# Kernel tuning notes

Hardware: AMD Instinct MI355X
Metric: run time of the kernel (lower is better)

## Reference

```python
import jax, jax.numpy as jnp
import numpy as np

# ---- static config ----
B, H, W, C = 32, 64, 64, 256
WS, SHIFT, NH = 8, 4, 8
HD = C // NH
N = WS * WS  # tokens per window
NW = (H // WS) * (W // WS)
EPS = 1e-5


def _relative_position_index(ws):
    ch, cw = np.meshgrid(np.arange(ws), np.arange(ws), indexing='ij')
    coords = np.stack([ch, cw]).reshape(2, -1)          # (2, N)
    rel = coords[:, :, None] - coords[:, None, :]        # (2, N, N)
    rel = rel.transpose(1, 2, 0)
    rel[:, :, 0] += ws - 1
    rel[:, :, 1] += ws - 1
    rel[:, :, 0] *= 2 * ws - 1
    return jnp.asarray(rel.sum(-1))                      # (N, N) int


def _shifted_window_mask(h, w, ws, shift):
    img = np.zeros((h, w))
    slices = (slice(0, -ws), slice(-ws, -shift), slice(-shift, None))
    cnt = 0
    for hs in slices:
        for wsl in slices:
            img[hs, wsl] = cnt
            cnt += 1
    mw = img.reshape(h // ws, ws, w // ws, ws).transpose(0, 2, 1, 3).reshape(-1, ws * ws)
    diff = mw[:, None, :] - mw[:, :, None]
    return jnp.asarray(np.where(diff != 0, -100.0, 0.0).astype(np.float32))  # (nW, N, N)


REL_IDX = _relative_position_index(WS)
ATTN_MASK = _shifted_window_mask(H, W, WS, SHIFT)


def _layernorm(x, g, b):
    mu = jnp.mean(x, axis=-1, keepdims=True)
    var = jnp.mean(jnp.square(x - mu), axis=-1, keepdims=True)
    return (x - mu) * jax.lax.rsqrt(var + EPS) * g + b


def _window_partition(x):  # (B,H,W,C) -> (B*nW, N, C)
    x = x.reshape(B, H // WS, WS, W // WS, WS, C)
    return x.transpose(0, 1, 3, 2, 4, 5).reshape(-1, N, C)


def _window_reverse(win):  # (B*nW, N, C) -> (B,H,W,C)
    x = win.reshape(B, H // WS, W // WS, WS, WS, C)
    return x.transpose(0, 1, 3, 2, 4, 5).reshape(B, H, W, C)


def setup_inputs() -> dict:
    key = jax.random.key(0)
    ks = jax.random.split(key, 6)
    s = lambda fan_in: 1.0 / np.sqrt(fan_in)
    return {
        'x': jax.random.normal(ks[0], (B, H * W, C), jnp.float32),
        'norm1_g': jnp.ones((C,), jnp.float32),
        'norm1_b': jnp.zeros((C,), jnp.float32),
        'qkv_w': jax.random.normal(ks[1], (C, 3 * C), jnp.float32) * s(C),
        'qkv_b': jnp.zeros((3 * C,), jnp.float32),
        'proj_w': jax.random.normal(ks[2], (C, C), jnp.float32) * s(C),
        'proj_b': jnp.zeros((C,), jnp.float32),
        'bias_table': jax.random.normal(ks[3], ((2 * WS - 1) ** 2, NH), jnp.float32) * 0.02,
        'norm2_g': jnp.ones((C,), jnp.float32),
        'norm2_b': jnp.zeros((C,), jnp.float32),
        'fc1_w': jax.random.normal(ks[4], (C, 4 * C), jnp.float32) * s(C),
        'fc1_b': jnp.zeros((4 * C,), jnp.float32),
        'fc2_w': jax.random.normal(ks[5], (4 * C, C), jnp.float32) * s(4 * C),
        'fc2_b': jnp.zeros((C,), jnp.float32),
    }


def reference(x, norm1_g, norm1_b, qkv_w, qkv_b, proj_w, proj_b, bias_table,
              norm2_g, norm2_b, fc1_w, fc1_b, fc2_w, fc2_b):
    shortcut = x
    h = _layernorm(x, norm1_g, norm1_b).reshape(B, H, W, C)
    # cyclic shift
    h = jnp.roll(h, shift=(-SHIFT, -SHIFT), axis=(1, 2))
    xw = _window_partition(h)                               # (Bw, N, C), Bw = B*nW
    # window attention
    qkv = xw @ qkv_w + qkv_b                                 # (Bw, N, 3C)
    qkv = qkv.reshape(-1, N, 3, NH, HD).transpose(2, 0, 3, 1, 4)
    q, k, v = qkv[0], qkv[1], qkv[2]                         # (Bw, NH, N, HD)
    attn = jnp.einsum('whnd,whmd->whnm', q * (HD ** -0.5), k)
    rpb = bias_table[REL_IDX.reshape(-1)].reshape(N, N, NH).transpose(2, 0, 1)
    attn = attn + rpb[None]
    attn = attn.reshape(B, NW, NH, N, N) + ATTN_MASK[None, :, None]
    attn = jax.nn.softmax(attn.reshape(-1, NH, N, N), axis=-1)
    out = jnp.einsum('whnm,whmd->whnd', attn, v)
    out = out.transpose(0, 2, 1, 3).reshape(-1, N, C)
    out = out @ proj_w + proj_b
    # reverse windows + shift back
    h = _window_reverse(out)
    h = jnp.roll(h, shift=(SHIFT, SHIFT), axis=(1, 2)).reshape(B, H * W, C)
    x = shortcut + h
    # MLP with pre-norm residual
    m = _layernorm(x, norm2_g, norm2_b)
    m = jax.nn.gelu(m @ fc1_w + fc1_b, approximate=False) @ fc2_w + fc2_b
    return x + m
```

## Files before the change

### kernel.cpp

```cpp
#include <hip/hip_runtime.h>
#include <hip/hip_bf16.h>


typedef __bf16 bf16;
typedef __bf16 bf16x8 __attribute__((ext_vector_type(8)));
typedef __bf16 bf16x4 __attribute__((ext_vector_type(4)));
typedef float  f32x4  __attribute__((ext_vector_type(4)));

#define M_TOK 131072

#define GLDS(gp, lp)                                                                   \
    __builtin_amdgcn_global_load_lds(                                                  \
        (const __attribute__((address_space(1))) unsigned int*)(gp),                   \
        (__attribute__((address_space(3))) unsigned int*)(lp), 16, 0, 0)

__global__ __launch_bounds__(256) void transpose_w(const float* __restrict__ src,
                                                   bf16* __restrict__ dst,
                                                   int K, int N) {
    int idx = blockIdx.x * 256 + threadIdx.x;
    int k = idx / N, n = idx - k * N;
    dst[(size_t)n * K + k] = (bf16)src[idx];
}

__global__ __launch_bounds__(256) void build_rpb(const float* __restrict__ bt,
                                                 float* __restrict__ rpb) {
    int idx = blockIdx.x * 256 + threadIdx.x;
    int h = idx >> 12, n = (idx >> 6) & 63, m = idx & 63;
    int ridx = ((n >> 3) - (m >> 3) + 7) * 15 + ((n & 7) - (m & 7) + 7);
    rpb[idx] = bt[ridx * 8 + h];
}

template <int PERM>
__global__ __launch_bounds__(256) void ln_k(const float* __restrict__ x,
                                            const float* __restrict__ g,
                                            const float* __restrict__ bb,
                                            bf16* __restrict__ dst) {
    int t = blockIdx.x * 4 + (threadIdx.x >> 6);
    int lane = threadIdx.x & 63;
    size_t src;
    if (PERM) {
        int w = t >> 6, n = t & 63;
        int b = w >> 6, nw = w & 63;
        int r = ((nw >> 3) * 8 + (n >> 3) + 4) & 63;
        int c = ((nw & 7) * 8 + (n & 7) + 4) & 63;
        src = ((size_t)b * 4096 + r * 64 + c) * 256;
    } else {
        src = (size_t)t * 256;
    }
    float4 v = *(const float4*)&x[src + lane * 4];
    float s = v.x + v.y + v.z + v.w;
    float sq = v.x * v.x + v.y * v.y + v.z * v.z + v.w * v.w;
#pragma unroll
    for (int off = 1; off < 64; off <<= 1) {
        s += __shfl_xor(s, off);
        sq += __shfl_xor(sq, off);
    }
    float mean = s * (1.0f / 256.0f);
    float var = sq * (1.0f / 256.0f) - mean * mean;
    float rstd = rsqrtf(var + 1e-5f);
    float4 gg = *(const float4*)&g[lane * 4];
    float4 bv = *(const float4*)&bb[lane * 4];
    bf16x4 o;
    o[0] = (bf16)((v.x - mean) * rstd * gg.x + bv.x);
    o[1] = (bf16)((v.y - mean) * rstd * gg.y + bv.y);
    o[2] = (bf16)((v.z - mean) * rstd * gg.z + bv.z);
    o[3] = (bf16)((v.w - mean) * rstd * gg.w + bv.w);
    *(bf16x4*)&dst[(size_t)t * 256 + lane * 4] = o;
}

__device__ __forceinline__ float fast_gelu(float v) {
    float t = v * v;
    float w = __builtin_fmaf(0.044715f * t, v, v);
    float e = __expf(-1.5957691216057308f * w);
    return v * __builtin_amdgcn_rcpf(1.0f + e);
}

template <int NDIM, int KDIM, int EPI>
__global__ __launch_bounds__(256) void gemm_k(const bf16* __restrict__ A,
                                              const bf16* __restrict__ Bt,
                                              const float* __restrict__ bias,
                                              bf16* __restrict__ outb,
                                              float* __restrict__ outf,
                                              const float* __restrict__ resid) {
    __shared__ __align__(16) bf16 SH[16384];
    constexpr int NBN = NDIM / 128;
    constexpr int NK = KDIM / 32;
    const int tid = threadIdx.x;
    const int nwg = gridDim.x;
    const int flat = blockIdx.x;
    const int cpx = nwg >> 3;
    const int orig = (flat & 7) * cpx + (flat >> 3);
    const int bm = orig / NBN, bn = orig % NBN;

    const int lane = tid & 63, wid = tid >> 6;
    const int wr = wid >> 1, wc = wid & 1;
    const int lhi = lane >> 4, llo = lane & 15;

    f32x4 acc[4][4];
#pragma unroll
    for (int i = 0; i < 4; i++)
#pragma unroll
        for (int j = 0; j < 4; j++) acc[i][j] = f32x4{0.f, 0.f, 0.f, 0.f};

    const int srow = wid * 32 + (lane >> 2);
    const int scol = (((lane & 3) - ((lane >> 3) & 3)) & 3) * 8;
    const bf16* Ap = A + (size_t)(bm * 128 + srow) * KDIM + scol;
    const bf16* Bp = Bt + (size_t)(bn * 128 + srow) * KDIM + scol;
    bf16* Al0 = SH + wid * 1024;
    bf16* Al1 = SH + 4096 + wid * 1024;
    bf16* Bl0 = SH + 8192 + wid * 1024;
    bf16* Bl1 = SH + 12288 + wid * 1024;
    const int gsw = ((lhi + (llo >> 1)) & 3) * 8;

#define STAGE(Adst, Bdst)                                                              \
    do {                                                                               \
        GLDS(Ap, (Adst));                                                              \
        GLDS(Ap + 16 * KDIM, (Adst) + 16 * 32);                                        \
        GLDS(Bp, (Bdst));                                                              \
        GLDS(Bp + 16 * KDIM, (Bdst) + 16 * 32);                                        \
        Ap += 32;                                                                      \
        Bp += 32;                                                                      \
    } while (0)

#define COMPUTE(buf)                                                                   \
    do {                                                                               \
        bf16x8 af[4], bfr[4];                                                          \
        _Pragma("unroll") for (int mi = 0; mi < 4; mi++) af[mi] =                      \
            *(const bf16x8*)&SH[(buf)*4096 + (wr * 64 + mi * 16 + llo) * 32 + gsw];    \
        _Pragma("unroll") for (int ni = 0; ni < 4; ni++) bfr[ni] =                     \
            *(const bf16x8*)&SH[8192 + (buf)*4096 + (wc * 64 + ni * 16 + llo) * 32 +   \
                                gsw];                                                  \
        _Pragma("unroll") for (int mi = 0; mi < 4; mi++)                               \
            _Pragma("unroll") for (int ni = 0; ni < 4; ni++) acc[mi][ni] =             \
                __builtin_amdgcn_mfma_f32_16x16x32_bf16(bfr[ni], af[mi],               \
                                                        acc[mi][ni], 0, 0, 0);         \
    } while (0)

#define WAIT_VM_N_BAR                                                                  \
    asm volatile("s_waitcnt vmcnt(4)" ::: "memory");                                   \
    __builtin_amdgcn_s_barrier();                                                      \
    __builtin_amdgcn_sched_barrier(0)

#define END_PHASE                                                                      \
    asm volatile("s_waitcnt lgkmcnt(0)" ::: "memory");                                 \
    __builtin_amdgcn_s_barrier();                                                      \
    __builtin_amdgcn_sched_barrier(0)

    STAGE(Al0, Bl0);
    for (int ks = 0; ks < NK - 2; ks += 2) {
        STAGE(Al1, Bl1);
        WAIT_VM_N_BAR;
        COMPUTE(0);
        END_PHASE;
        STAGE(Al0, Bl0);
        WAIT_VM_N_BAR;
        COMPUTE(1);
        END_PHASE;
    }
    STAGE(Al1, Bl1);
    WAIT_VM_N_BAR;
    COMPUTE(0);
    asm volatile("s_waitcnt vmcnt(0)" ::: "memory");
    __builtin_amdgcn_s_barrier();
    __builtin_amdgcn_sched_barrier(0);
    COMPUTE(1);

#undef STAGE
#undef COMPUTE
#undef WAIT_VM_N_BAR
#undef END_PHASE

    __syncthreads();

    char* shb = (char*)SH;
    if constexpr (EPI == 0 || EPI == 2) {
#pragma unroll
        for (int ni = 0; ni < 4; ni++) {
            const int lcol = wc * 64 + ni * 16 + lhi * 4;
            const float4 b4 = *(const float4*)&bias[bn * 128 + lcol];
#pragma unroll
            for (int mi = 0; mi < 4; mi++) {
                const int ltok = wr * 64 + mi * 16 + llo;
                float v0 = acc[mi][ni][0] + b4.x;
                float v1 = acc[mi][ni][1] + b4.y;
                float v2 = acc[mi][ni][2] + b4.z;
                float v3 = acc[mi][ni][3] + b4.w;
                bf16x4 o;
                if constexpr (EPI == 2) {
                    o[0] = (bf16)fast_gelu(v0); o[1] = (bf16)fast_gelu(v1);
                    o[2] = (bf16)fast_gelu(v2); o[3] = (bf16)fast_gelu(v3);
                } else {
                    o[0] = (bf16)v0; o[1] = (bf16)v1; o[2] = (bf16)v2; o[3] = (bf16)v3;
                }
                const int u2 = (lcol >> 3) ^ (ltok & 15);
                *(bf16x4*)(shb + ltok * 256 + u2 * 16 + (lcol & 7) * 2) = o;
            }
        }
        __syncthreads();
        const int j = lane & 15;
#pragma unroll
        for (int rnd = 0; rnd < 8; rnd++) {
            const int ltok = wid * 32 + rnd * 4 + (lane >> 4);
            const int u2 = j ^ (ltok & 15);
            bf16x8 v = *(const bf16x8*)(shb + ltok * 256 + u2 * 16);
            *(bf16x8*)&outb[(size_t)(bm * 128 + ltok) * NDIM + bn * 128 + j * 8] = v;
        }
    } else {
#pragma unroll
        for (int p = 0; p < 2; p++) {
            if (wc == p) {
#pragma unroll
                for (int ni = 0; ni < 4; ni++) {
                    const int lcolh = ni * 16 + lhi * 4;
                    const float4 b4 = *(const float4*)&bias[bn * 128 + p * 64 + lcolh];
#pragma unroll
                    for (int mi = 0; mi < 4; mi++) {
                        const int ltok = wr * 64 + mi * 16 + llo;
                        float4 o = {acc[mi][ni][0] + b4.x, acc[mi][ni][1] + b4.y,
                                    acc[mi][ni][2] + b4.z, acc[mi][ni][3] + b4.w};
                        const int u2 = (lcolh >> 2) ^ (ltok & 15);
                        *(float4*)(shb + ltok * 256 + u2 * 16) = o;
                    }
                }
            }
            __syncthreads();
            const int j = lane & 15;
#pragma unroll
            for (int rnd = 0; rnd < 8; rnd++) {
                const int ltok = wid * 32 + rnd * 4 + (lane >> 4);
                const int u2 = j ^ (ltok & 15);
                float4 v = *(const float4*)(shb + ltok * 256 + u2 * 16);
                const int gcol = bn * 128 + p * 64 + j * 4;
                const int grow = bm * 128 + ltok;
                if constexpr (EPI == 1) {
                    int w = grow >> 6, n = grow & 63;
                    int b = w >> 6, nw = w & 63;
                    int rr = ((nw >> 3) * 8 + (n >> 3) + 4) & 63;
                    int cc = ((nw & 7) * 8 + (n & 7) + 4) & 63;
                    size_t dst = ((size_t)b * 4096 + rr * 64 + cc) * 256 + gcol;
                    float4 rs = *(const float4*)&resid[dst];
                    float4 o = {rs.x + v.x, rs.y + v.y, rs.z + v.z, rs.w + v.w};
                    *(float4*)&outf[dst] = o;
                } else {
                    size_t dst = (size_t)grow * NDIM + gcol;
                    float4 cur = *(const float4*)&outf[dst];
                    float4 o = {cur.x + v.x, cur.y + v.y, cur.z + v.z, cur.w + v.w};
                    *(float4*)&outf[dst] = o;
                }
            }
            if (p == 0) __syncthreads();
        }
    }
}

__device__ __forceinline__ int regid3(int p) { return p < 56 ? 0 : (p < 60 ? 1 : 2); }

__global__ __launch_bounds__(256) void attn_k(const bf16* __restrict__ qkv,
                                              const float* __restrict__ rpb,
                                              bf16* __restrict__ aout) {
    __shared__ __align__(16) bf16 Pl[4][64 * 80];
    const int wid = threadIdx.x >> 6, lane = threadIdx.x & 63;
    const int lhi = lane >> 4, llo = lane & 15;
    const int wh = blockIdx.x * 4 + wid;
    const int w = wh >> 3, h = wh & 7;
    const bf16* base = qkv + (size_t)w * (64 * 768);

    bf16x8 qf[4], kf[4];
#pragma unroll
    for (int i = 0; i < 4; i++)
        qf[i] = *(const bf16x8*)(base + (i * 16 + llo) * 768 + h * 32 + lhi * 8);
#pragma unroll
    for (int i = 0; i < 4; i++)
        kf[i] = *(const bf16x8*)(base + (i * 16 + llo) * 768 + 256 + h * 32 + lhi * 8);
    f32x4 s[4][4];
#pragma unroll
    for (int mi = 0; mi < 4; mi++)
#pragma unroll
        for (int ni = 0; ni < 4; ni++) {
            s[mi][ni] = f32x4{0.f, 0.f, 0.f, 0.f};
            s[mi][ni] =
                __builtin_amdgcn_mfma_f32_16x16x32_bf16(qf[mi], kf[ni], s[mi][ni], 0, 0, 0);
        }

    const int nw = w & 63;
    const int pr0 = (nw >> 3) * 8, pc0 = (nw & 7) * 8;
    int creg[4];
#pragma unroll
    for (int ni = 0; ni < 4; ni++) {
        int m = ni * 16 + llo;
        creg[ni] = regid3(pr0 + (m >> 3)) * 3 + regid3(pc0 + (m & 7));
    }
    float rmax[4][4], rsum[4][4];
#pragma unroll
    for (int mi = 0; mi < 4; mi++)
#pragma unroll
        for (int r = 0; r < 4; r++) {
            int n = mi * 16 + lhi * 4 + r;
            int rreg = regid3(pr0 + (n >> 3)) * 3 + regid3(pc0 + (n & 7));
            float mx = -1e30f;
#pragma unroll
            for (int ni = 0; ni < 4; ni++) {
                int m = ni * 16 + llo;
                float sv = s[mi][ni][r] * 0.17677669529663687f + rpb[(h * 64 + n) * 64 + m] +
                           (rreg == creg[ni] ? 0.0f : -100.0f);
                s[mi][ni][r] = sv;
                mx = fmaxf(mx, sv);
            }
            rmax[mi][r] = mx;
        }
#pragma unroll
    for (int off = 1; off < 16; off <<= 1)
#pragma unroll
        for (int mi = 0; mi < 4; mi++)
#pragma unroll
            for (int r = 0; r < 4; r++)
                rmax[mi][r] = fmaxf(rmax[mi][r], __shfl_xor(rmax[mi][r], off));
#pragma unroll
    for (int mi = 0; mi < 4; mi++)
#pragma unroll
        for (int r = 0; r < 4; r++) {
            float a = 0.f;
#pragma unroll
            for (int ni = 0; ni < 4; ni++) {
                float p = __expf(s[mi][ni][r] - rmax[mi][r]);
                s[mi][ni][r] = p;
                a += p;
            }
            rsum[mi][r] = a;
        }
#pragma unroll
    for (int off = 1; off < 16; off <<= 1)
#pragma unroll
        for (int mi = 0; mi < 4; mi++)
#pragma unroll
            for (int r = 0; r < 4; r++) rsum[mi][r] += __shfl_xor(rsum[mi][r], off);

    bf16* P = Pl[wid];
#pragma unroll
    for (int mi = 0; mi < 4; mi++)
#pragma unroll
        for (int r = 0; r < 4; r++) {
            float rinv = 1.0f / rsum[mi][r];
            int row = mi * 16 + lhi * 4 + r;
#pragma unroll
            for (int ni = 0; ni < 4; ni++)
                P[row * 80 + ni * 16 + llo] = (bf16)(s[mi][ni][r] * rinv);
        }

    f32x4 o[4][2];
#pragma unroll
    for (int mi = 0; mi < 4; mi++)
#pragma unroll
        for (int ni = 0; ni < 2; ni++) o[mi][ni] = f32x4{0.f, 0.f, 0.f, 0.f};
#pragma unroll
    for (int kc = 0; kc < 2; kc++) {
        bf16x8 pf[4], vf[2];
#pragma unroll
        for (int mi = 0; mi < 4; mi++)
            pf[mi] = *(const bf16x8*)(P + (mi * 16 + llo) * 80 + kc * 32 + lhi * 8);
#pragma unroll
        for (int ni = 0; ni < 2; ni++)
#pragma unroll
            for (int j = 0; j < 8; j++)
                vf[ni][j] = base[(kc * 32 + lhi * 8 + j) * 768 + 512 + h * 32 + ni * 16 + llo];
#pragma unroll
        for (int mi = 0; mi < 4; mi++)
#pragma unroll
            for (int ni = 0; ni < 2; ni++)
                o[mi][ni] =
                    __builtin_amdgcn_mfma_f32_16x16x32_bf16(pf[mi], vf[ni], o[mi][ni], 0, 0, 0);
    }
#pragma unroll
    for (int mi = 0; mi < 4; mi++)
#pragma unroll
        for (int ni = 0; ni < 2; ni++)
#pragma unroll
            for (int r = 0; r < 4; r++) {
                int row = mi * 16 + lhi * 4 + r;
                aout[(size_t)(w * 64 + row) * 256 + h * 32 + ni * 16 + llo] =
                    (bf16)o[mi][ni][r];
            }
}

extern "C" void kernel_launch(void* const* d_in, const int* in_sizes, int n_in,
                              void* d_out, int out_size, void* d_ws, size_t ws_size,
                              hipStream_t stream) {
    const float* x      = (const float*)d_in[0];
    const float* n1g    = (const float*)d_in[1];
    const float* n1b    = (const float*)d_in[2];
    const float* qkv_w  = (const float*)d_in[3];
    const float* qkv_b  = (const float*)d_in[4];
    const float* proj_w = (const float*)d_in[5];
    const float* proj_b = (const float*)d_in[6];
    const float* btab   = (const float*)d_in[7];
    const float* n2g    = (const float*)d_in[8];
    const float* n2b    = (const float*)d_in[9];
    const float* fc1_w  = (const float*)d_in[10];
    const float* fc1_b  = (const float*)d_in[11];
    const float* fc2_w  = (const float*)d_in[12];
    const float* fc2_b  = (const float*)d_in[13];
    float* out = (float*)d_out;
    char* ws = (char*)d_ws;

    constexpr size_t o_xw   = 0;
    constexpr size_t o_qkv  = 67108864ull;
    constexpr size_t o_attn = 268435456ull;
    constexpr size_t o_g    = 0;
    constexpr size_t o_h    = 268435456ull;
    constexpr size_t o_wq   = 335544320ull;
    constexpr size_t o_wp   = o_wq + 393216;
    constexpr size_t o_w1   = o_wp + 131072;
    constexpr size_t o_w2   = o_w1 + 524288;
    constexpr size_t o_rpb  = o_w2 + 524288;

    bf16* XW   = (bf16*)(ws + o_xw);
    bf16* QKV  = (bf16*)(ws + o_qkv);
    bf16* ATTN = (bf16*)(ws + o_attn);
    bf16* G    = (bf16*)(ws + o_g);
    bf16* Hb   = (bf16*)(ws + o_h);
    bf16* WQ   = (bf16*)(ws + o_wq);
    bf16* WP   = (bf16*)(ws + o_wp);
    bf16* W1   = (bf16*)(ws + o_w1);
    bf16* W2   = (bf16*)(ws + o_w2);
    float* RPB = (float*)(ws + o_rpb);

    dim3 blk(256);
    transpose_w<<<768, blk, 0, stream>>>(qkv_w, WQ, 256, 768);
    transpose_w<<<256, blk, 0, stream>>>(proj_w, WP, 256, 256);
    transpose_w<<<1024, blk, 0, stream>>>(fc1_w, W1, 256, 1024);
    transpose_w<<<1024, blk, 0, stream>>>(fc2_w, W2, 1024, 256);
    build_rpb<<<128, blk, 0, stream>>>(btab, RPB);

    ln_k<1><<<M_TOK / 4, blk, 0, stream>>>(x, n1g, n1b, XW);
    gemm_k<768, 256, 0><<<6 * 1024, blk, 0, stream>>>(XW, WQ, qkv_b, QKV, nullptr, nullptr);
    attn_k<<<4096, blk, 0, stream>>>(QKV, RPB, ATTN);
    gemm_k<256, 256, 1><<<2 * 1024, blk, 0, stream>>>(ATTN, WP, proj_b, nullptr, out, x);
    ln_k<0><<<M_TOK / 4, blk, 0, stream>>>(out, n2g, n2b, Hb);
    gemm_k<1024, 256, 2><<<8 * 1024, blk, 0, stream>>>(Hb, W1, fc1_b, G, nullptr, nullptr);
    gemm_k<256, 1024, 3><<<2 * 1024, blk, 0, stream>>>(G, W2, fc2_b, nullptr, out, nullptr);
}
```

Measured before the change: 615.9 us.

## Deepen GEMM LDS pipeline from double to triple buffering

Changes the GEMM main loop from a two-stage to a three-stage global-to-LDS prefetch pipeline, issuing two K-steps ahead and waiting with vmcnt(8). This is meant to hide more global load latency behind MFMA work. The cost is a larger LDS footprint (48KB instead of 32KB), which may reduce occupancy, and a runtime buffer index in place of fixed unrolled buffers.

```diff
diff --git a/kernel.cpp b/kernel.cpp
--- a/kernel.cpp
+++ b/kernel.cpp
@@ -82,9 +82,10 @@
                                               bf16* __restrict__ outb,
                                               float* __restrict__ outf,
                                               const float* __restrict__ resid) {
-    __shared__ __align__(16) bf16 SH[16384];
+    __shared__ __align__(16) bf16 SH[24576];
     constexpr int NBN = NDIM / 128;
     constexpr int NK = KDIM / 32;
+    static_assert(NK >= 3, "pipeline needs >=3 K-steps");
     const int tid = threadIdx.x;
     const int nwg = gridDim.x;
     const int flat = blockIdx.x;
@@ -106,38 +107,36 @@
     const int scol = (((lane & 3) - ((lane >> 3) & 3)) & 3) * 8;
     const bf16* Ap = A + (size_t)(bm * 128 + srow) * KDIM + scol;
     const bf16* Bp = Bt + (size_t)(bn * 128 + srow) * KDIM + scol;
-    bf16* Al0 = SH + wid * 1024;
-    bf16* Al1 = SH + 4096 + wid * 1024;
-    bf16* Bl0 = SH + 8192 + wid * 1024;
-    bf16* Bl1 = SH + 12288 + wid * 1024;
     const int gsw = ((lhi + (llo >> 1)) & 3) * 8;
 
-#define STAGE(Adst, Bdst)                                                              \
+#define STAGE(bufidx)                                                                  \
     do {                                                                               \
-        GLDS(Ap, (Adst));                                                              \
-        GLDS(Ap + 16 * KDIM, (Adst) + 16 * 32);                                        \
-        GLDS(Bp, (Bdst));                                                              \
-        GLDS(Bp + 16 * KDIM, (Bdst) + 16 * 32);                                        \
+        bf16* Al = SH + (bufidx)*4096 + wid * 1024;                                    \
+        bf16* Bl = SH + 12288 + (bufidx)*4096 + wid * 1024;                            \
+        GLDS(Ap, Al);                                                                  \
+        GLDS(Ap + 16 * KDIM, Al + 16 * 32);                                            \
+        GLDS(Bp, Bl);                                                                  \
+        GLDS(Bp + 16 * KDIM, Bl + 16 * 32);                                            \
         Ap += 32;                                                                      \
         Bp += 32;                                                                      \
     } while (0)
 
-#define COMPUTE(buf)                                                                   \
+#define COMPUTE(bufidx)                                                                \
     do {                                                                               \
+        const int ab = (bufidx)*4096;                                                  \
         bf16x8 af[4], bfr[4];                                                          \
         _Pragma("unroll") for (int mi = 0; mi < 4; mi++) af[mi] =                      \
-            *(const bf16x8*)&SH[(buf)*4096 + (wr * 64 + mi * 16 + llo) * 32 + gsw];    \
+            *(const bf16x8*)&SH[ab + (wr * 64 + mi * 16 + llo) * 32 + gsw];            \
         _Pragma("unroll") for (int ni = 0; ni < 4; ni++) bfr[ni] =                     \
-            *(const bf16x8*)&SH[8192 + (buf)*4096 + (wc * 64 + ni * 16 + llo) * 32 +   \
-                                gsw];                                                  \
+            *(const bf16x8*)&SH[12288 + ab + (wc * 64 + ni * 16 + llo) * 32 + gsw];    \
         _Pragma("unroll") for (int mi = 0; mi < 4; mi++)                               \
             _Pragma("unroll") for (int ni = 0; ni < 4; ni++) acc[mi][ni] =             \
                 __builtin_amdgcn_mfma_f32_16x16x32_bf16(bfr[ni], af[mi],               \
                                                         acc[mi][ni], 0, 0, 0);         \
     } while (0)
 
-#define WAIT_VM_N_BAR                                                                  \
-    asm volatile("s_waitcnt vmcnt(4)" ::: "memory");                                   \
+#define WAITBAR(N)                                                                     \
+    asm volatile("s_waitcnt vmcnt(" #N ")" ::: "memory");                              \
     __builtin_amdgcn_s_barrier();                                                      \
     __builtin_amdgcn_sched_barrier(0)
 
@@ -146,28 +145,29 @@
     __builtin_amdgcn_s_barrier();                                                      \
     __builtin_amdgcn_sched_barrier(0)
 
-    STAGE(Al0, Bl0);
-    for (int ks = 0; ks < NK - 2; ks += 2) {
-        STAGE(Al1, Bl1);
-        WAIT_VM_N_BAR;
-        COMPUTE(0);
+    STAGE(0);
+    STAGE(1);
+    STAGE(2);
+    int buf = 0;
+    for (int i = 0; i + 3 < NK; ++i) {
+        WAITBAR(8);
+        COMPUTE(buf);
         END_PHASE;
-        STAGE(Al0, Bl0);
-        WAIT_VM_N_BAR;
-        COMPUTE(1);
-        END_PHASE;
-    }
-    STAGE(Al1, Bl1);
-    WAIT_VM_N_BAR;
-    COMPUTE(0);
-    asm volatile("s_waitcnt vmcnt(0)" ::: "memory");
-    __builtin_amdgcn_s_barrier();
-    __builtin_amdgcn_sched_barrier(0);
-    COMPUTE(1);
+        STAGE(buf);
+        buf = (buf == 2) ? 0 : buf + 1;
+    }
+    WAITBAR(8);
+    COMPUTE(buf);
+    buf = (buf == 2) ? 0 : buf + 1;
+    WAITBAR(4);
+    COMPUTE(buf);
+    buf = (buf == 2) ? 0 : buf + 1;
+    WAITBAR(0);
+    COMPUTE(buf);
 
 #undef STAGE
 #undef COMPUTE
-#undef WAIT_VM_N_BAR
+#undef WAITBAR
 #undef END_PHASE
 
     __syncthreads();
```

Measured after the change: 604.1 us. No clear change (-1.9%).

## Load GEMM operand fragments directly from global memory into registers

Applied to the files above, without the earlier changes.

Replaces the LDS-staged, double-buffered global_load_lds pipeline in the GEMM main loop with direct per-wave global loads of MFMA fragments into registers, prefetching the next K-slice while computing the current one. This removes LDS traffic and the per-step barriers. In exchange, each tile row is fetched separately by every wave that uses it (the A tile twice, the B tile twice), with no sharing through LDS. The 16-byte global loads per lane are also strided across rows, which lowers coalescing and relies on L1/L2 hits.

```diff
diff --git a/kernel.cpp b/kernel.cpp
--- a/kernel.cpp
+++ b/kernel.cpp
@@ -8,11 +8,6 @@
 typedef float  f32x4  __attribute__((ext_vector_type(4)));
 
 #define M_TOK 131072
-
-#define GLDS(gp, lp)                                                                   \
-    __builtin_amdgcn_global_load_lds(                                                  \
-        (const __attribute__((address_space(1))) unsigned int*)(gp),                   \
-        (__attribute__((address_space(3))) unsigned int*)(lp), 16, 0, 0)
 
 __global__ __launch_bounds__(256) void transpose_w(const float* __restrict__ src,
                                                    bf16* __restrict__ dst,
@@ -102,76 +97,43 @@
 #pragma unroll
         for (int j = 0; j < 4; j++) acc[i][j] = f32x4{0.f, 0.f, 0.f, 0.f};
 
-    const int srow = wid * 32 + (lane >> 2);
-    const int scol = (((lane & 3) - ((lane >> 3) & 3)) & 3) * 8;
-    const bf16* Ap = A + (size_t)(bm * 128 + srow) * KDIM + scol;
-    const bf16* Bp = Bt + (size_t)(bn * 128 + srow) * KDIM + scol;
-    bf16* Al0 = SH + wid * 1024;
-    bf16* Al1 = SH + 4096 + wid * 1024;
-    bf16* Bl0 = SH + 8192 + wid * 1024;
-    bf16* Bl1 = SH + 12288 + wid * 1024;
-    const int gsw = ((lhi + (llo >> 1)) & 3) * 8;
-
-#define STAGE(Adst, Bdst)                                                              \
-    do {                                                                               \
-        GLDS(Ap, (Adst));                                                              \
-        GLDS(Ap + 16 * KDIM, (Adst) + 16 * 32);                                        \
-        GLDS(Bp, (Bdst));                                                              \
-        GLDS(Bp + 16 * KDIM, (Bdst) + 16 * 32);                                        \
-        Ap += 32;                                                                      \
-        Bp += 32;                                                                      \
-    } while (0)
-
-#define COMPUTE(buf)                                                                   \
-    do {                                                                               \
-        bf16x8 af[4], bfr[4];                                                          \
-        _Pragma("unroll") for (int mi = 0; mi < 4; mi++) af[mi] =                      \
-            *(const bf16x8*)&SH[(buf)*4096 + (wr * 64 + mi * 16 + llo) * 32 + gsw];    \
-        _Pragma("unroll") for (int ni = 0; ni < 4; ni++) bfr[ni] =                     \
-            *(const bf16x8*)&SH[8192 + (buf)*4096 + (wc * 64 + ni * 16 + llo) * 32 +   \
-                                gsw];                                                  \
-        _Pragma("unroll") for (int mi = 0; mi < 4; mi++)                               \
-            _Pragma("unroll") for (int ni = 0; ni < 4; ni++) acc[mi][ni] =             \
-                __builtin_amdgcn_mfma_f32_16x16x32_bf16(bfr[ni], af[mi],               \
-                                                        acc[mi][ni], 0, 0, 0);         \
-    } while (0)
-
-#define WAIT_VM_N_BAR                                                                  \
-    asm volatile("s_waitcnt vmcnt(4)" ::: "memory");                                   \
-    __builtin_amdgcn_s_barrier();                                                      \
-    __builtin_amdgcn_sched_barrier(0)
-
-#define END_PHASE                                                                      \
-    asm volatile("s_waitcnt lgkmcnt(0)" ::: "memory");                                 \
-    __builtin_amdgcn_s_barrier();                                                      \
-    __builtin_amdgcn_sched_barrier(0)
-
-    STAGE(Al0, Bl0);
-    for (int ks = 0; ks < NK - 2; ks += 2) {
-        STAGE(Al1, Bl1);
-        WAIT_VM_N_BAR;
-        COMPUTE(0);
-        END_PHASE;
-        STAGE(Al0, Bl0);
-        WAIT_VM_N_BAR;
-        COMPUTE(1);
-        END_PHASE;
-    }
-    STAGE(Al1, Bl1);
-    WAIT_VM_N_BAR;
-    COMPUTE(0);
-    asm volatile("s_waitcnt vmcnt(0)" ::: "memory");
-    __builtin_amdgcn_s_barrier();
-    __builtin_amdgcn_sched_barrier(0);
-    COMPUTE(1);
-
-#undef STAGE
-#undef COMPUTE
-#undef WAIT_VM_N_BAR
-#undef END_PHASE
+    const bf16* Aw = A + (size_t)(bm * 128 + wr * 64 + llo) * KDIM + lhi * 8;
+    const bf16* Bw = Bt + (size_t)(bn * 128 + wc * 64 + llo) * KDIM + lhi * 8;
+
+    bf16x8 afc[4], bfc[4];
+#pragma unroll
+    for (int mi = 0; mi < 4; mi++)
+        afc[mi] = *(const bf16x8*)(Aw + mi * 16 * KDIM);
+#pragma unroll
+    for (int ni = 0; ni < 4; ni++)
+        bfc[ni] = *(const bf16x8*)(Bw + ni * 16 * KDIM);
+
+#pragma unroll
+    for (int ks = 0; ks < NK; ks++) {
+        bf16x8 afn[4], bfn[4];
+        if (ks + 1 < NK) {
+#pragma unroll
+            for (int mi = 0; mi < 4; mi++)
+                afn[mi] = *(const bf16x8*)(Aw + (ks + 1) * 32 + mi * 16 * KDIM);
+#pragma unroll
+            for (int ni = 0; ni < 4; ni++)
+                bfn[ni] = *(const bf16x8*)(Bw + (ks + 1) * 32 + ni * 16 * KDIM);
+        }
+#pragma unroll
+        for (int mi = 0; mi < 4; mi++)
+#pragma unroll
+            for (int ni = 0; ni < 4; ni++)
+                acc[mi][ni] = __builtin_amdgcn_mfma_f32_16x16x32_bf16(bfc[ni], afc[mi],
+                                                                      acc[mi][ni], 0, 0, 0);
+        if (ks + 1 < NK) {
+#pragma unroll
+            for (int mi = 0; mi < 4; mi++) afc[mi] = afn[mi];
+#pragma unroll
+            for (int ni = 0; ni < 4; ni++) bfc[ni] = bfn[ni];
+        }
+    }
 
     __syncthreads();
-
     char* shb = (char*)SH;
     if constexpr (EPI == 0 || EPI == 2) {
 #pragma unroll
```

Result: slower. 1.011 ms (+64.1%).
